# Performance work log

Measured on AMD Instinct MI355X. Metric: run time of the kernel, lower is better.

Reference implementation:

```python
import jax, jax.numpy as jnp
import numpy as np

B, S, C = 4, 2048, 1024

def setup_inputs() -> dict:
    key = jax.random.key(0)
    ks = jax.random.split(key, 9)
    lim = 1.0 / np.sqrt(C)  # torch nn.Linear default init range
    def lin_params(kw, kb):
        W = jax.random.uniform(kw, (C, C), jnp.float32, -lim, lim)
        b = jax.random.uniform(kb, (C,), jnp.float32, -lim, lim)
        return W, b
    Wq, bq = lin_params(ks[0], ks[1])
    Wk, bk = lin_params(ks[2], ks[3])
    Wv, bv = lin_params(ks[4], ks[5])
    query = jax.random.normal(ks[6], (B, S, C), jnp.float32)
    key_t = jax.random.normal(ks[7], (B, S, C), jnp.float32)
    value = jax.random.normal(ks[8], (B, S, C), jnp.float32)
    return {"query": query, "key": key_t, "value": value,
            "Wq": Wq, "bq": bq, "Wk": Wk, "bk": bk, "Wv": Wv, "bv": bv}

def reference(query, key, value, Wq, bq, Wk, bk, Wv, bv):
    # Linear projections: y = x @ W^T + b (torch Linear convention, W is [out, in])
    Q = jnp.einsum('bsc,dc->bsd', query, Wq) + bq
    K = jnp.einsum('bsc,dc->bsd', key, Wk) + bk
    V = jnp.einsum('bsc,dc->bsd', value, Wv) + bv
    scale = jnp.float32(C) ** 0.5
    scores = jnp.einsum('bqd,bkd->bqk', Q, K) / scale  # [B, S, S]
    attn = jax.nn.softmax(scores, axis=-1)
    out = jnp.einsum('bqk,bkd->bqd', attn, V)  # [B, S, C]
    return out
```

## Files before the change

kernel.cpp:

```cpp
#include <hip/hip_runtime.h>
#include <hip/hip_bf16.h>


typedef _Float16 half8 __attribute__((ext_vector_type(8)));
typedef _Float16 half4 __attribute__((ext_vector_type(4)));
typedef float f32x4 __attribute__((ext_vector_type(4)));

#define AS1(p) ((const __attribute__((address_space(1))) void*)(p))
#define AS3(p) ((__attribute__((address_space(3))) void*)(p))
#define MFMA16(a, b, c) __builtin_amdgcn_mfma_f32_16x16x32_f16(a, b, c, 0, 0, 0)

__global__ __launch_bounds__(256) void cvt6_f32_f16(
    const float* __restrict__ q, const float* __restrict__ k,
    const float* __restrict__ v, const float* __restrict__ wq,
    const float* __restrict__ wk, const float* __restrict__ wv,
    _Float16* __restrict__ Xq, _Float16* __restrict__ Wqh) {
    constexpr long XSZ = 8388608, WSZ = 1048576;
    const int b = blockIdx.x;
    const float* s;
    _Float16* d;
    long i;
    if (b < 12288) {
        const int tz = b >> 12;
        s = tz == 0 ? q : tz == 1 ? k : v;
        d = Xq + (long)tz * XSZ;
        i = (long)(b & 4095) * 2048 + threadIdx.x * 8;
    } else {
        const int b2 = b - 12288;
        const int tz = b2 >> 9;
        s = tz == 0 ? wq : tz == 1 ? wk : wv;
        d = Wqh + (long)tz * WSZ;
        i = (long)(b2 & 511) * 2048 + threadIdx.x * 8;
    }
    float4 a = *(const float4*)(s + i);
    float4 c = *(const float4*)(s + i + 4);
    half8 h;
    h[0] = (_Float16)a.x; h[1] = (_Float16)a.y; h[2] = (_Float16)a.z; h[3] = (_Float16)a.w;
    h[4] = (_Float16)c.x; h[5] = (_Float16)c.y; h[6] = (_Float16)c.z; h[7] = (_Float16)c.w;
    *(half8*)(d + i) = h;
}

template <int K, int NX_SH, int R, int NYT_SH, bool BIAS, bool F16OUT, bool PROJ3>
__global__ __launch_bounds__(256, 2)
void gemm_nt(const _Float16* __restrict__ A, const _Float16* __restrict__ Bt,
             const float* __restrict__ b0, const float* __restrict__ b1,
             const float* __restrict__ b2, void* __restrict__ Cout,
             _Float16* __restrict__ VtOut, int N, float scale,
             long sA, long sB, long sC) {
    __shared__ _Float16 Asm[128 * 128] __attribute__((aligned(16)));
    __shared__ _Float16 Bsm[128 * 128] __attribute__((aligned(16)));
    const int tid = threadIdx.x;
    const int lane = tid & 63;
    const int wave = tid >> 6;

    const int lin = blockIdx.x;
    const int g = lin & 7;
    const int s = lin >> 3;
    const int xt = s & ((1 << NX_SH) - 1);
    const int row_id = g * R + (s >> NX_SH);
    const int yt = row_id & ((1 << NYT_SH) - 1);
    const int tz = row_id >> NYT_SH;
    const int m0 = yt * 128;
    const int n0 = xt * 128;

    const float* bias = nullptr;
    if constexpr (PROJ3) {
        A += (long)tz * 8388608;
        Bt += (long)tz * 1048576;
        bias = tz == 0 ? b0 : tz == 1 ? b1 : b2;
    } else {
        A += (long)tz * sA;
        Bt += (long)tz * sB;
    }

    const int rin = lane >> 4;
    const int pch = lane & 15;
    const int quad = lane >> 4;
    const int l16 = lane & 15;
    const int wm = (wave >> 1) << 6;
    const int wn = (wave & 1) << 6;
    const int fa_base = (wm + l16) * 128;
    const int fb_base = (wn + l16) * 128;
    int ch[4];
#pragma unroll
    for (int ks = 0; ks < 4; ++ks) ch[ks] = (((ks * 4 + quad) ^ l16) << 3);

    f32x4 acc[4][4];
#pragma unroll
    for (int i = 0; i < 4; i++)
#pragma unroll
        for (int j = 0; j < 4; j++)
#pragma unroll
            for (int r = 0; r < 4; r++) acc[i][j][r] = 0.0f;

    const _Float16* Abase = A + (long)m0 * K;
    const _Float16* Bbase = Bt + (long)n0 * K;

    for (int k0 = 0; k0 < K; k0 += 128) {
        __syncthreads();
#pragma unroll
        for (int u = 0; u < 16; ++u) {
            const int t = wave + u * 4;
            const int sl = t & 31;
            const int r = sl * 4 + rin;
            const int lq = (pch ^ (((sl & 3) << 2) + rin)) << 3;
            if (t < 32) {
                __builtin_amdgcn_global_load_lds(
                    AS1(Abase + (long)r * K + k0 + lq),
                    AS3(Asm + sl * 512), 16, 0, 0);
            } else {
                __builtin_amdgcn_global_load_lds(
                    AS1(Bbase + (long)r * K + k0 + lq),
                    AS3(Bsm + sl * 512), 16, 0, 0);
            }
        }
        __syncthreads();

#pragma unroll
        for (int ks = 0; ks < 4; ++ks) {
            half8 af[4], bf[4];
#pragma unroll
            for (int i = 0; i < 4; i++) af[i] = *(const half8*)(Asm + fa_base + i * 2048 + ch[ks]);
#pragma unroll
            for (int j = 0; j < 4; j++) bf[j] = *(const half8*)(Bsm + fb_base + j * 2048 + ch[ks]);
#pragma unroll
            for (int i = 0; i < 4; i++)
#pragma unroll
                for (int j = 0; j < 4; j++)
                    acc[i][j] = MFMA16(af[i], bf[j], acc[i][j]);
        }
    }

    const bool trout = PROJ3 && tz == 2;
#pragma unroll
    for (int i = 0; i < 4; i++) {
        const int row = m0 + wm + i * 16 + quad * 4;
#pragma unroll
        for (int j = 0; j < 4; j++) {
            const int col = n0 + wn + j * 16 + l16;
            const float badd = BIAS ? bias[col] : 0.0f;
            if (trout) {
                const long b = row >> 11;
                const int sl = row & 2047;
                half4 h;
#pragma unroll
                for (int r = 0; r < 4; r++) h[r] = (_Float16)(acc[i][j][r] * scale + badd);
                *(half4*)(VtOut + b * 2097152 + (long)col * 2048 + sl) = h;
            } else if constexpr (PROJ3) {
                _Float16* o = (_Float16*)Cout + (long)tz * 8388608;
#pragma unroll
                for (int r = 0; r < 4; r++)
                    o[(long)(row + r) * N + col] = (_Float16)(acc[i][j][r] * scale + badd);
            } else {
#pragma unroll
                for (int r = 0; r < 4; r++) {
                    float v = acc[i][j][r] * scale + badd;
                    if constexpr (F16OUT)
                        ((_Float16*)Cout + (long)tz * sC)[(long)(row + r) * N + col] = (_Float16)v;
                    else
                        ((float*)Cout + (long)tz * sC)[(long)(row + r) * N + col] = v;
                }
            }
        }
    }
}

__global__ __launch_bounds__(256) void softmax_f16(const _Float16* __restrict__ S,
                                                   _Float16* __restrict__ P) {
    const long row = blockIdx.x;
    const int t = threadIdx.x;
    const int wave = t >> 6, lane = t & 63;
    half8 h = ((const half8*)(S + row * 2048))[t];
    float v[8];
#pragma unroll
    for (int j = 0; j < 8; j++) v[j] = (float)h[j];
    float m = v[0];
#pragma unroll
    for (int j = 1; j < 8; j++) m = fmaxf(m, v[j]);
#pragma unroll
    for (int off = 32; off > 0; off >>= 1) m = fmaxf(m, __shfl_xor(m, off, 64));
    __shared__ float redm[4], reds[4];
    if (lane == 0) redm[wave] = m;
    __syncthreads();
    m = fmaxf(fmaxf(redm[0], redm[1]), fmaxf(redm[2], redm[3]));
    float sum = 0.0f;
#pragma unroll
    for (int j = 0; j < 8; j++) { v[j] = __expf(v[j] - m); sum += v[j]; }
#pragma unroll
    for (int off = 32; off > 0; off >>= 1) sum += __shfl_xor(sum, off, 64);
    if (lane == 0) reds[wave] = sum;
    __syncthreads();
    sum = (reds[0] + reds[1]) + (reds[2] + reds[3]);
    const float inv = 1.0f / sum;
    half8 o;
#pragma unroll
    for (int j = 0; j < 8; j++) o[j] = (_Float16)(v[j] * inv);
    ((half8*)(P + row * 2048))[t] = o;
}

extern "C" void kernel_launch(void* const* d_in, const int* in_sizes, int n_in,
                              void* d_out, int out_size, void* d_ws, size_t ws_size,
                              hipStream_t stream) {
    constexpr int B = 4, S = 2048, C = 1024;
    constexpr long XSZ = (long)B * S * C;
    constexpr long WSZ = (long)C * C;

    const float* query = (const float*)d_in[0];
    const float* key   = (const float*)d_in[1];
    const float* value = (const float*)d_in[2];
    const float* Wq = (const float*)d_in[3];
    const float* bq = (const float*)d_in[4];
    const float* Wk = (const float*)d_in[5];
    const float* bk = (const float*)d_in[6];
    const float* Wv = (const float*)d_in[7];
    const float* bv = (const float*)d_in[8];
    float* out = (float*)d_out;
    char* ws = (char*)d_ws;

    _Float16* Xq  = (_Float16*)(ws + 0);
    _Float16* Wqh = (_Float16*)(ws + 3 * XSZ * 2);
    _Float16* scores = (_Float16*)(ws + 0);
    _Float16* Qh  = (_Float16*)(ws + 73400320);
    _Float16* attn = (_Float16*)(ws + 73400320);
    _Float16* Vt  = (_Float16*)(ws + 106954752);
    if (ws_size < 123731968) return;

    cvt6_f32_f16<<<13824, 256, 0, stream>>>(
        query, key, value, Wq, Wk, Wv, Xq, Wqh);

    gemm_nt<1024, 3, 24, 6, true, true, true><<<1536, 256, 0, stream>>>(
        Xq, Wqh, bq, bk, bv, Qh, Vt, C, 1.0f, 0, 0, 0);

    gemm_nt<1024, 4, 8, 4, false, true, false><<<1024, 256, 0, stream>>>(
        Qh, Qh + XSZ, nullptr, nullptr, nullptr, scores, nullptr, S, 0.03125f,
        (long)S * C, (long)S * C, (long)S * S);

    softmax_f16<<<B * S, 256, 0, stream>>>(scores, attn);

    gemm_nt<2048, 3, 8, 4, false, false, false><<<512, 256, 0, stream>>>(
        attn, Vt, nullptr, nullptr, nullptr, out, nullptr, C, 1.0f,
        (long)S * S, (long)C * S, (long)S * C);
}
```

Baseline: 298.2 us.

## Fuse fp32-to-fp16 activation conversion into QKV projection GEMM loads

```diff
diff --git a/kernel.cpp b/kernel.cpp
--- a/kernel.cpp
+++ b/kernel.cpp
@@ -10,28 +10,15 @@
 #define AS3(p) ((__attribute__((address_space(3))) void*)(p))
 #define MFMA16(a, b, c) __builtin_amdgcn_mfma_f32_16x16x32_f16(a, b, c, 0, 0, 0)
 
-__global__ __launch_bounds__(256) void cvt6_f32_f16(
-    const float* __restrict__ q, const float* __restrict__ k,
-    const float* __restrict__ v, const float* __restrict__ wq,
-    const float* __restrict__ wk, const float* __restrict__ wv,
-    _Float16* __restrict__ Xq, _Float16* __restrict__ Wqh) {
-    constexpr long XSZ = 8388608, WSZ = 1048576;
+__global__ __launch_bounds__(256) void cvtw_f32_f16(
+    const float* __restrict__ wq, const float* __restrict__ wk,
+    const float* __restrict__ wv, _Float16* __restrict__ Wqh) {
+    constexpr long WSZ = 1048576;
     const int b = blockIdx.x;
-    const float* s;
-    _Float16* d;
-    long i;
-    if (b < 12288) {
-        const int tz = b >> 12;
-        s = tz == 0 ? q : tz == 1 ? k : v;
-        d = Xq + (long)tz * XSZ;
-        i = (long)(b & 4095) * 2048 + threadIdx.x * 8;
-    } else {
-        const int b2 = b - 12288;
-        const int tz = b2 >> 9;
-        s = tz == 0 ? wq : tz == 1 ? wk : wv;
-        d = Wqh + (long)tz * WSZ;
-        i = (long)(b2 & 511) * 2048 + threadIdx.x * 8;
-    }
+    const int tz = b >> 9;
+    const float* s = tz == 0 ? wq : tz == 1 ? wk : wv;
+    _Float16* d = Wqh + (long)tz * WSZ;
+    const long i = (long)(b & 511) * 2048 + threadIdx.x * 8;
     float4 a = *(const float4*)(s + i);
     float4 c = *(const float4*)(s + i + 4);
     half8 h;
@@ -40,12 +27,134 @@
     *(half8*)(d + i) = h;
 }
 
-template <int K, int NX_SH, int R, int NYT_SH, bool BIAS, bool F16OUT, bool PROJ3>
+__global__ __launch_bounds__(256, 2)
+void gemm_proj_a32(const float* __restrict__ X0, const float* __restrict__ X1,
+                   const float* __restrict__ X2, const _Float16* __restrict__ Wh,
+                   const float* __restrict__ b0, const float* __restrict__ b1,
+                   const float* __restrict__ b2, _Float16* __restrict__ QKout,
+                   _Float16* __restrict__ VtOut) {
+    constexpr int K = 1024;
+    __shared__ float AsmF[128 * 64] __attribute__((aligned(16)));
+    __shared__ _Float16 Bsm[128 * 64] __attribute__((aligned(16)));
+    const int tid = threadIdx.x;
+    const int lane = tid & 63;
+    const int wave = tid >> 6;
+
+    const int lin = blockIdx.x;
+    const int g = lin & 7;
+    const int s = lin >> 3;
+    const int xt = s & 7;
+    const int row_id = g * 24 + (s >> 3);
+    const int yt = row_id & 63;
+    const int tz = row_id >> 6;
+    const int m0 = yt * 128;
+    const int n0 = xt * 128;
+
+    const float* Xp = tz == 0 ? X0 : tz == 1 ? X1 : X2;
+    const float* bias = tz == 0 ? b0 : tz == 1 ? b1 : b2;
+    const float* Abase = Xp + (long)m0 * K;
+    const _Float16* Bbase = Wh + (long)tz * 1048576 + (long)n0 * K;
+
+    const int rin = lane >> 4;
+    const int pch = lane & 15;
+    const int srow8 = lane >> 3;
+    const int sq = ((lane & 7) ^ srow8) << 3;
+    const int quad = lane >> 4;
+    const int l16 = lane & 15;
+    const int wm = (wave >> 1) << 6;
+    const int wn = (wave & 1) << 6;
+    const int fa_base = (wm + l16) * 64;
+    const int fb_base = (wn + l16) * 64;
+    int chB[2];
+#pragma unroll
+    for (int ks = 0; ks < 2; ++ks) chB[ks] = ((ks * 4 + quad) ^ (l16 & 7)) << 3;
+    int chA0[2], chA1[2];
+#pragma unroll
+    for (int ks = 0; ks < 2; ++ks) {
+        const int f = ks * 4 + quad;
+        chA0[ks] = ((2 * f) ^ l16) << 2;
+        chA1[ks] = ((2 * f + 1) ^ l16) << 2;
+    }
+
+    f32x4 acc[4][4];
+#pragma unroll
+    for (int i = 0; i < 4; i++)
+#pragma unroll
+        for (int j = 0; j < 4; j++)
+#pragma unroll
+            for (int r = 0; r < 4; r++) acc[i][j][r] = 0.0f;
+
+    for (int k0 = 0; k0 < K; k0 += 64) {
+        __syncthreads();
+#pragma unroll
+        for (int u = 0; u < 8; ++u) {
+            const int sl = wave + u * 4;
+            const int r = sl * 4 + rin;
+            const int lq = (pch ^ (r & 15)) << 2;
+            __builtin_amdgcn_global_load_lds(
+                AS1(Abase + (long)r * K + k0 + lq),
+                AS3(AsmF + sl * 256), 16, 0, 0);
+        }
+#pragma unroll
+        for (int u = 0; u < 4; ++u) {
+            const int t = wave + u * 4;
+            __builtin_amdgcn_global_load_lds(
+                AS1(Bbase + (long)(t * 8 + srow8) * K + k0 + sq),
+                AS3(Bsm + t * 512), 16, 0, 0);
+        }
+        __syncthreads();
+
+#pragma unroll
+        for (int ks = 0; ks < 2; ++ks) {
+            half8 af[4], bf[4];
+#pragma unroll
+            for (int i = 0; i < 4; i++) {
+                const f32x4 lo = *(const f32x4*)(AsmF + fa_base + i * 1024 + chA0[ks]);
+                const f32x4 hi = *(const f32x4*)(AsmF + fa_base + i * 1024 + chA1[ks]);
+                af[i][0] = (_Float16)lo[0]; af[i][1] = (_Float16)lo[1];
+                af[i][2] = (_Float16)lo[2]; af[i][3] = (_Float16)lo[3];
+                af[i][4] = (_Float16)hi[0]; af[i][5] = (_Float16)hi[1];
+                af[i][6] = (_Float16)hi[2]; af[i][7] = (_Float16)hi[3];
+            }
+#pragma unroll
+            for (int j = 0; j < 4; j++) bf[j] = *(const half8*)(Bsm + fb_base + j * 1024 + chB[ks]);
+#pragma unroll
+            for (int i = 0; i < 4; i++)
+#pragma unroll
+                for (int j = 0; j < 4; j++)
+                    acc[i][j] = MFMA16(af[i], bf[j], acc[i][j]);
+        }
+    }
+
+    const bool trout = (tz == 2);
+#pragma unroll
+    for (int i = 0; i < 4; i++) {
+        const int row = m0 + wm + i * 16 + quad * 4;
+#pragma unroll
+        for (int j = 0; j < 4; j++) {
+            const int col = n0 + wn + j * 16 + l16;
+            const float badd = bias[col];
+            if (trout) {
+                const long b = row >> 11;
+                const int sl = row & 2047;
+                half4 h;
+#pragma unroll
+                for (int r = 0; r < 4; r++) h[r] = (_Float16)(acc[i][j][r] + badd);
+                *(half4*)(VtOut + b * 2097152 + (long)col * 2048 + sl) = h;
+            } else {
+                _Float16* o = QKout + (long)tz * 8388608;
+#pragma unroll
+                for (int r = 0; r < 4; r++)
+                    o[(long)(row + r) * 1024 + col] = (_Float16)(acc[i][j][r] + badd);
+            }
+        }
+    }
+}
+
+template <int K, int NX_SH, int R, int NYT_SH, bool F16OUT>
 __global__ __launch_bounds__(256, 2)
 void gemm_nt(const _Float16* __restrict__ A, const _Float16* __restrict__ Bt,
-             const float* __restrict__ b0, const float* __restrict__ b1,
-             const float* __restrict__ b2, void* __restrict__ Cout,
-             _Float16* __restrict__ VtOut, int N, float scale,
+             void* __restrict__ Cout, int N, float scale,
              long sA, long sB, long sC) {
     __shared__ _Float16 Asm[128 * 128] __attribute__((aligned(16)));
     __shared__ _Float16 Bsm[128 * 128] __attribute__((aligned(16)));
@@ -63,15 +172,8 @@
     const int m0 = yt * 128;
     const int n0 = xt * 128;
 
-    const float* bias = nullptr;
-    if constexpr (PROJ3) {
-        A += (long)tz * 8388608;
-        Bt += (long)tz * 1048576;
-        bias = tz == 0 ? b0 : tz == 1 ? b1 : b2;
-    } else {
-        A += (long)tz * sA;
-        Bt += (long)tz * sB;
-    }
+    A += (long)tz * sA;
+    Bt += (long)tz * sB;
 
     const int rin = lane >> 4;
     const int pch = lane & 15;
@@ -131,35 +233,19 @@
         }
     }
 
-    const bool trout = PROJ3 && tz == 2;
 #pragma unroll
     for (int i = 0; i < 4; i++) {
         const int row = m0 + wm + i * 16 + quad * 4;
 #pragma unroll
         for (int j = 0; j < 4; j++) {
             const int col = n0 + wn + j * 16 + l16;
-            const float badd = BIAS ? bias[col] : 0.0f;
-            if (trout) {
-                const long b = row >> 11;
-                const int sl = row & 2047;
-                half4 h;
-#pragma unroll
-                for (int r = 0; r < 4; r++) h[r] = (_Float16)(acc[i][j][r] * scale + badd);
-                *(half4*)(VtOut + b * 2097152 + (long)col * 2048 + sl) = h;
-            } else if constexpr (PROJ3) {
-                _Float16* o = (_Float16*)Cout + (long)tz * 8388608;
-#pragma unroll
-                for (int r = 0; r < 4; r++)
-                    o[(long)(row + r) * N + col] = (_Float16)(acc[i][j][r] * scale + badd);
-            } else {
-#pragma unroll
-                for (int r = 0; r < 4; r++) {
-                    float v = acc[i][j][r] * scale + badd;
-                    if constexpr (F16OUT)
-                        ((_Float16*)Cout + (long)tz * sC)[(long)(row + r) * N + col] = (_Float16)v;
-                    else
-                        ((float*)Cout + (long)tz * sC)[(long)(row + r) * N + col] = v;
-                }
+#pragma unroll
+            for (int r = 0; r < 4; r++) {
+                float v = acc[i][j][r] * scale;
+                if constexpr (F16OUT)
+                    ((_Float16*)Cout + (long)tz * sC)[(long)(row + r) * N + col] = (_Float16)v;
+                else
+                    ((float*)Cout + (long)tz * sC)[(long)(row + r) * N + col] = v;
             }
         }
     }
@@ -203,7 +289,6 @@
                               hipStream_t stream) {
     constexpr int B = 4, S = 2048, C = 1024;
     constexpr long XSZ = (long)B * S * C;
-    constexpr long WSZ = (long)C * C;
 
     const float* query = (const float*)d_in[0];
     const float* key   = (const float*)d_in[1];
@@ -217,27 +302,25 @@
     float* out = (float*)d_out;
     char* ws = (char*)d_ws;
 
-    _Float16* Xq  = (_Float16*)(ws + 0);
-    _Float16* Wqh = (_Float16*)(ws + 3 * XSZ * 2);
+    _Float16* Wqh = (_Float16*)(ws + 50331648);
     _Float16* scores = (_Float16*)(ws + 0);
     _Float16* Qh  = (_Float16*)(ws + 73400320);
     _Float16* attn = (_Float16*)(ws + 73400320);
     _Float16* Vt  = (_Float16*)(ws + 106954752);
     if (ws_size < 123731968) return;
 
-    cvt6_f32_f16<<<13824, 256, 0, stream>>>(
-        query, key, value, Wq, Wk, Wv, Xq, Wqh);
-
-    gemm_nt<1024, 3, 24, 6, true, true, true><<<1536, 256, 0, stream>>>(
-        Xq, Wqh, bq, bk, bv, Qh, Vt, C, 1.0f, 0, 0, 0);
-
-    gemm_nt<1024, 4, 8, 4, false, true, false><<<1024, 256, 0, stream>>>(
-        Qh, Qh + XSZ, nullptr, nullptr, nullptr, scores, nullptr, S, 0.03125f,
+    cvtw_f32_f16<<<1536, 256, 0, stream>>>(Wq, Wk, Wv, Wqh);
+
+    gemm_proj_a32<<<1536, 256, 0, stream>>>(
+        query, key, value, Wqh, bq, bk, bv, Qh, Vt);
+
+    gemm_nt<1024, 4, 8, 4, true><<<1024, 256, 0, stream>>>(
+        Qh, Qh + XSZ, scores, S, 0.03125f,
         (long)S * C, (long)S * C, (long)S * S);
 
     softmax_f16<<<B * S, 256, 0, stream>>>(scores, attn);
 
-    gemm_nt<2048, 3, 8, 4, false, false, false><<<512, 256, 0, stream>>>(
-        attn, Vt, nullptr, nullptr, nullptr, out, nullptr, C, 1.0f,
+    gemm_nt<2048, 3, 8, 4, false><<<512, 256, 0, stream>>>(
+        attn, Vt, out, C, 1.0f,
         (long)S * S, (long)C * S, (long)S * C);
 }
```

New measurement: 309.3 us. 3.7% more time.
